# Optimization experiments

Hardware: AMD Instinct MI355X
Metric: run time of the kernel (lower is better)

The kernel has to match this reference:

```python
import jax, jax.numpy as jnp
import numpy as np

B = 16384
D = 64            # bottom_mlp_layers[-1] = embedding_dim
DENSE = 512
HIST = 50         # history length per row
C_CAMP = 1000     # num_collisions for campaign table (sqrt(1e6))
C_FEAT = 316      # num_collisions for 1e5-vocab tables
NQ_CAMP = 1000    # ceil(1e6/1000)
NQ_FEAT = 317     # ceil(1e5/316)
NFEAT = 7
N = NFEAT + 1 + 1 # sparse features + dense row
PROJ = 128


def setup_inputs() -> dict:
    key = jax.random.key(0)
    ks = jax.random.split(key, 20)
    inp = {
        'x': jax.random.normal(ks[0], (B, DENSE), jnp.float32),
        'hist_idx': jax.random.randint(ks[1], (B * HIST,), 0, 1000000),
        'hist_offsets': jnp.arange(B, dtype=jnp.int64) * HIST,
        'feat_idx': jax.random.randint(ks[2], (B, NFEAT), 0, 100000),
        # QR embedding tables (quotient, remainder)
        'Wq_c': jax.random.normal(ks[3], (NQ_CAMP, D), jnp.float32) * 0.05,
        'Wr_c': jax.random.normal(ks[4], (C_CAMP, D), jnp.float32) * 0.05,
        'Wq_f': jax.random.normal(ks[5], (NFEAT, NQ_FEAT, D), jnp.float32) * 0.05,
        'Wr_f': jax.random.normal(ks[6], (NFEAT, C_FEAT, D), jnp.float32) * 0.05,
        # bottom MLP: 512->512 relu 512->256 relu 256->64
        'W0': jax.random.normal(ks[7], (512, DENSE), jnp.float32) * 0.03,
        'b0': jnp.zeros((512,), jnp.float32),
        'W1': jax.random.normal(ks[8], (256, 512), jnp.float32) * 0.04,
        'b1': jnp.zeros((256,), jnp.float32),
        'W2': jax.random.normal(ks[9], (64, 256), jnp.float32) * 0.06,
        'b2': jnp.zeros((64,), jnp.float32),
        # projection: (D + (N^2-N)/2) -> PROJ ; 64 + 36 = 100
        'Wp': jax.random.normal(ks[10], (PROJ, D + (N * N - N) // 2), jnp.float32) * 0.1,
        'bp': jnp.zeros((PROJ,), jnp.float32),
    }
    return inp


def _forward(x, hist_idx, hist_offsets, feat_idx, Wq_c, Wr_c, Wq_f, Wr_f,
             W0, b0, W1, b1, W2, b2, Wp, bp):
    # bottom MLP
    h = jax.nn.relu(x @ W0.T + b0)
    h = jax.nn.relu(h @ W1.T + b1)
    dense = h @ W2.T + b2                                   # [B, D]

    # QR embedding bag (mode='mean', operation='mult') for history feature
    e = Wq_c[hist_idx // C_CAMP] * Wr_c[hist_idx % C_CAMP]  # [M, D]
    M = hist_idx.shape[0]
    seg = jnp.cumsum(jnp.zeros((M,), jnp.int32).at[hist_offsets].add(1)) - 1
    sums = jax.ops.segment_sum(e, seg, num_segments=B)      # [B, D]
    counts = jnp.diff(jnp.concatenate([hist_offsets, jnp.array([M], hist_offsets.dtype)]))
    hist_emb = sums / counts[:, None].astype(sums.dtype)

    # single-valued QR lookups (bag size 1 -> mean == lookup)
    t = jnp.arange(NFEAT)[None, :]
    fe = Wq_f[t, feat_idx // C_FEAT] * Wr_f[t, feat_idx % C_FEAT]  # [B, NFEAT, D]

    # pairwise dot interaction: upper triangle (offset=1) of T @ T^T
    T = jnp.concatenate([dense[:, None, :], hist_emb[:, None, :], fe], axis=1)  # [B, N, D]
    Z = jnp.einsum('bnd,bmd->bnm', T, T)
    row, col = np.triu_indices(N, k=1)
    Z_flat = Z[:, row, col]                                  # [B, (N^2-N)/2]

    combined = jnp.concatenate([dense, Z_flat], axis=1)
    return combined @ Wp.T + bp                              # [B, PROJ]


def reference(x, hist_idx, hist_offsets, feat_idx, Wq_c, Wr_c, Wq_f, Wr_f,
              W0, b0, W1, b1, W2, b2, Wp, bp):
    return _forward(x, hist_idx, hist_offsets, feat_idx, Wq_c, Wr_c, Wq_f, Wr_f,
                    W0, b0, W1, b1, W2, b2, Wp, bp)
```

## Files before the change

### kernel.cpp

```cpp
#include <hip/hip_runtime.h>
#include <hip/hip_bf16.h>
#include <stdint.h>

#define DENSE_D 512
#define HIDDEN1 512
#define HIDDEN2 256
#define EMB_D   64
#define NFEAT   7
#define NROWS   9
#define NPAIRS  36
#define COMB    100
#define KPROJ   128
#define PROJ    128
#define C_CAMP  1000
#define C_FEAT  316
#define NQ_FEAT 317
#define TROWS   16
#define GROWS   8
#define HISTMAX 64

typedef __attribute__((ext_vector_type(8)))  __bf16 bf16x8;
typedef __attribute__((ext_vector_type(8)))  unsigned short ushort8;
typedef __attribute__((ext_vector_type(4)))  float  facc4;

#define GLD_LDS16(gp, lp) __builtin_amdgcn_global_load_lds( \
    (__attribute__((address_space(1))) void*)(gp), \
    (__attribute__((address_space(3))) void*)(lp), 16, 0, 0)

__device__ inline unsigned short f2bf(float f) {
    __hip_bfloat16 h = __float2bfloat16(f);
    return *reinterpret_cast<unsigned short*>(&h);
}
__device__ inline float blo(unsigned int u) { return __uint_as_float(u << 16); }
__device__ inline float bhi(unsigned int u) { return __uint_as_float(u & 0xffff0000u); }

template<int BM, int BN, int BK, int WM, int WN, bool RELU, bool A_F32>
__global__ __launch_bounds__(WM * WN * 64)
void gemm16(const void* __restrict__ Avoid,
            const unsigned short* __restrict__ W,
            const float* __restrict__ bias,
            unsigned short* __restrict__ Cout,
            int M, int N, int K)
{
    constexpr int THREADS = WM * WN * 64;
    constexpr int MREP    = BM / (WM * 16);
    constexpr int NREP    = BN / (WN * 16);
    constexpr int SUB     = BK / 32;
    constexpr int ACH     = BM * BK / 8;
    constexpr int BCH     = BN * BK / 8;

    __shared__ __align__(16) unsigned short Asm[BK / 8][BM][8];
    __shared__ __align__(16) unsigned short Bsm[BK / 8][BN][8];

    const int tid  = threadIdx.x;
    const int lane = tid & 63;
    const int wave = tid >> 6;
    const int wm   = wave / WN;
    const int wn   = wave % WN;
    const int row0 = blockIdx.x * BM;
    const int col0 = blockIdx.y * BN;
    const int fr   = lane & 15;
    const int fk   = lane >> 4;

    facc4 acc[MREP][NREP] = {};

    for (int k0 = 0; k0 < K; k0 += BK) {
        if (A_F32) {
            const float* Af = (const float*)Avoid;
            #pragma unroll
            for (int it = 0; it < ACH / THREADS; ++it) {
                const int p  = it * THREADS + tid;
                const int r  = p & (BM - 1);
                const int kc = p / BM;
                const float* src = Af + (size_t)(row0 + r) * K + k0 + kc * 8;
                const float4 v0 = *reinterpret_cast<const float4*>(src);
                const float4 v1 = *reinterpret_cast<const float4*>(src + 4);
                ushort8 cv;
                cv[0] = f2bf(v0.x); cv[1] = f2bf(v0.y);
                cv[2] = f2bf(v0.z); cv[3] = f2bf(v0.w);
                cv[4] = f2bf(v1.x); cv[5] = f2bf(v1.y);
                cv[6] = f2bf(v1.z); cv[7] = f2bf(v1.w);
                *reinterpret_cast<ushort8*>(
                    (unsigned short*)(&Asm[0][0][0]) + (size_t)p * 8) = cv;
            }
        } else {
            const unsigned short* Ab = (const unsigned short*)Avoid;
            #pragma unroll
            for (int it = 0; it < ACH / THREADS; ++it) {
                const int p  = it * THREADS + tid;
                const int r  = p & (BM - 1);
                const int kc = p / BM;
                GLD_LDS16(Ab + (size_t)(row0 + r) * K + k0 + kc * 8,
                          (&Asm[0][0][0]) + (size_t)p * 8);
            }
        }
        #pragma unroll
        for (int it = 0; it < BCH / THREADS; ++it) {
            const int p  = it * THREADS + tid;
            const int r  = p & (BN - 1);
            const int kc = p / BN;
            GLD_LDS16(W + (size_t)(col0 + r) * K + k0 + kc * 8,
                      (&Bsm[0][0][0]) + (size_t)p * 8);
        }
        __syncthreads();

        #pragma unroll
        for (int s = 0; s < SUB; ++s) {
            bf16x8 af[MREP], bw[NREP];
            #pragma unroll
            for (int m = 0; m < MREP; ++m)
                af[m] = *reinterpret_cast<const bf16x8*>(
                    &Asm[s * 4 + fk][wm * (MREP * 16) + m * 16 + fr][0]);
            #pragma unroll
            for (int n = 0; n < NREP; ++n)
                bw[n] = *reinterpret_cast<const bf16x8*>(
                    &Bsm[s * 4 + fk][wn * (NREP * 16) + n * 16 + fr][0]);
            #pragma unroll
            for (int m = 0; m < MREP; ++m)
                #pragma unroll
                for (int n = 0; n < NREP; ++n)
                    acc[m][n] = __builtin_amdgcn_mfma_f32_16x16x32_bf16(
                        af[m], bw[n], acc[m][n], 0, 0, 0);
        }
        __syncthreads();
    }

    #pragma unroll
    for (int n = 0; n < NREP; ++n) {
        const int col = col0 + wn * (NREP * 16) + n * 16 + fr;
        const float bv = bias[col];
        #pragma unroll
        for (int m = 0; m < MREP; ++m) {
            #pragma unroll
            for (int j = 0; j < 4; ++j) {
                const int row = row0 + wm * (MREP * 16) + m * 16 + fk * 4 + j;
                float v = acc[m][n][j] + bv;
                if (RELU) v = fmaxf(v, 0.f);
                Cout[(size_t)row * N + col] = f2bf(v);
            }
        }
    }
}

__device__ inline void cast_seg(const float* __restrict__ src,
                                unsigned short* __restrict__ dst,
                                int n4, int id, int stride)
{
    for (int i = id; i < n4; i += stride) {
        const float4 v = reinterpret_cast<const float4*>(src)[i];
        ushort4 o;
        o.x = f2bf(v.x); o.y = f2bf(v.y); o.z = f2bf(v.z); o.w = f2bf(v.w);
        reinterpret_cast<ushort4*>(dst)[i] = o;
    }
}

__global__ __launch_bounds__(256)
void prep_all(const float* __restrict__ W0, const float* __restrict__ W1,
              const float* __restrict__ W2, const float* __restrict__ Wp,
              const float* __restrict__ Wq_c, const float* __restrict__ Wr_c,
              const float* __restrict__ Wq_f, const float* __restrict__ Wr_f,
              unsigned short* w0b, unsigned short* w1b, unsigned short* w2b,
              unsigned short* wpb, unsigned short* qcb, unsigned short* rcb,
              unsigned short* qfb, unsigned short* rfb)
{
    const int id = blockIdx.x * blockDim.x + threadIdx.x;
    const int stride = gridDim.x * blockDim.x;
    cast_seg(W0,   w0b, HIDDEN1 * DENSE_D / 4,   id, stride);
    cast_seg(W1,   w1b, HIDDEN2 * HIDDEN1 / 4,   id, stride);
    cast_seg(W2,   w2b, EMB_D * HIDDEN2 / 4,     id, stride);
    cast_seg(Wq_c, qcb, C_CAMP * EMB_D / 4,      id, stride);
    cast_seg(Wr_c, rcb, C_CAMP * EMB_D / 4,      id, stride);
    cast_seg(Wq_f, qfb, NFEAT * NQ_FEAT * EMB_D / 4, id, stride);
    cast_seg(Wr_f, rfb, NFEAT * C_FEAT * EMB_D / 4,  id, stride);
    for (int i = id; i < PROJ * KPROJ; i += stride) {
        const int r = i >> 7, c = i & 127;
        wpb[i] = (c < COMB) ? f2bf(Wp[r * COMB + c]) : (unsigned short)0;
    }
}

__global__ __launch_bounds__(256)
void hist_gather(const int* __restrict__ hist_idx,
                 const int* __restrict__ hist_off,
                 const unsigned short* __restrict__ qcb,
                 const unsigned short* __restrict__ rcb,
                 unsigned short* __restrict__ hemb,
                 int B, int Mtot)
{
    const int r0 = blockIdx.x * GROWS;
    const int t  = threadIdx.x;

    __shared__ int2 soff[GROWS][HISTMAX];
    __shared__ int  scnt[GROWS];

    for (int p = t; p < GROWS * HISTMAX; p += 256) {
        const int row = p >> 6;
        const int i   = p & 63;
        const int br  = r0 + row;
        const int start = hist_off[br];
        const int end   = (br + 1 < B) ? hist_off[br + 1] : Mtot;
        const int cnt   = end - start;
        int2 o = make_int2(0, 0);
        if (i < cnt) {
            const int hi = hist_idx[start + i];
            const int q = hi / C_CAMP;
            o = make_int2(q * EMB_D, (hi - q * C_CAMP) * EMB_D);
        }
        soff[row][i] = o;
        if (i == 0) scnt[row] = cnt;
    }
    __syncthreads();

    const int lane = t & 63;
    const int wv   = t >> 6;
    const int half = lane >> 5;
    const int row  = wv * 2 + half;
    const int l5   = lane & 31;
    const int slot = l5 >> 3;
    const int d8   = l5 & 7;
    const int cnt  = scnt[row];

    const unsigned short* qb = qcb + d8 * 8;
    const unsigned short* rb = rcb + d8 * 8;

    float a[8] = {};
    #define ACC8(q, r) do { \
        a[0] += blo((q).x) * blo((r).x); a[1] += bhi((q).x) * bhi((r).x); \
        a[2] += blo((q).y) * blo((r).y); a[3] += bhi((q).y) * bhi((r).y); \
        a[4] += blo((q).z) * blo((r).z); a[5] += bhi((q).z) * bhi((r).z); \
        a[6] += blo((q).w) * blo((r).w); a[7] += bhi((q).w) * bhi((r).w); } while (0)

    const int full = cnt >> 2;
    int g = 0;
    for (; g + 4 <= full; g += 4) {
        int2 o[4];
        #pragma unroll
        for (int j = 0; j < 4; ++j) o[j] = soff[row][(g + j) * 4 + slot];
        uint4 uq[4], ur[4];
        #pragma unroll
        for (int j = 0; j < 4; ++j) {
            uq[j] = *reinterpret_cast<const uint4*>(qb + o[j].x);
            ur[j] = *reinterpret_cast<const uint4*>(rb + o[j].y);
        }
        #pragma unroll
        for (int j = 0; j < 4; ++j) ACC8(uq[j], ur[j]);
    }
    for (; g < full; ++g) {
        const int2 o = soff[row][g * 4 + slot];
        const uint4 uq = *reinterpret_cast<const uint4*>(qb + o.x);
        const uint4 ur = *reinterpret_cast<const uint4*>(rb + o.y);
        ACC8(uq, ur);
    }
    {
        const int idx = (full << 2) + slot;
        const int2 o = soff[row][idx & (HISTMAX - 1)];
        const uint4 uq = *reinterpret_cast<const uint4*>(qb + o.x);
        const uint4 ur = *reinterpret_cast<const uint4*>(rb + o.y);
        if (idx < cnt) ACC8(uq, ur);
    }
    #undef ACC8

    #pragma unroll
    for (int k = 0; k < 8; ++k) {
        a[k] += __shfl_xor(a[k], 8);
        a[k] += __shfl_xor(a[k], 16);
    }

    if (slot == 0) {
        const float inv = 1.f / (float)max(cnt, 1);
        union { unsigned short s[8]; uint4 u; } pk;
        #pragma unroll
        for (int k = 0; k < 8; ++k) pk.s[k] = f2bf(a[k] * inv);
        *reinterpret_cast<uint4*>(hemb + (size_t)(r0 + row) * EMB_D + d8 * 8) = pk.u;
    }
}

__global__ __launch_bounds__(256)
void tail_rest(const unsigned short* __restrict__ h1b,
               const unsigned short* __restrict__ w2b,
               const float* __restrict__ b2,
               const unsigned short* __restrict__ hemb,
               const int* __restrict__ feat_idx,
               const unsigned short* __restrict__ qfb,
               const unsigned short* __restrict__ rfb,
               const unsigned short* __restrict__ wpb,
               const float* __restrict__ bp,
               float* __restrict__ out)
{
    const int r0   = blockIdx.x * TROWS;
    const int t    = threadIdx.x;
    const int lane = t & 63;
    const int wave = t >> 6;
    const int fr   = lane & 15;
    const int fk   = lane >> 4;

    __shared__ __align__(16) unsigned short T[TROWS][NROWS][72];
    __shared__ __align__(16) unsigned short combs[TROWS][136];

    {
        facc4 acc = {};
        const unsigned short* arow = h1b + (size_t)(r0 + fr) * HIDDEN2;
        const unsigned short* brow = w2b + (size_t)(wave * 16 + fr) * HIDDEN2;
        #pragma unroll
        for (int kw = 0; kw < 8; ++kw) {
            const bf16x8 af = *reinterpret_cast<const bf16x8*>(arow + kw * 32 + fk * 8);
            const bf16x8 bw = *reinterpret_cast<const bf16x8*>(brow + kw * 32 + fk * 8);
            acc = __builtin_amdgcn_mfma_f32_16x16x32_bf16(af, bw, acc, 0, 0, 0);
        }
        const int col = wave * 16 + fr;
        const float bv = b2[col];
        #pragma unroll
        for (int j = 0; j < 4; ++j) {
            const int row = fk * 4 + j;
            const unsigned short hv = f2bf(acc[j] + bv);
            T[row][0][col]  = hv;
            combs[row][col] = hv;
        }
    }

    for (int p = t; p < TROWS * 18; p += 256) {
        const int row = p / 18, c = p % 18;
        *reinterpret_cast<unsigned int*>(&combs[row][100 + c * 2]) = 0u;
    }

    if (t < TROWS * 8) {
        const int row = t >> 3, o8 = t & 7;
        const uint4 v = *reinterpret_cast<const uint4*>(
            hemb + (size_t)(r0 + row) * EMB_D + o8 * 8);
        *reinterpret_cast<uint4*>(&T[row][1][o8 * 8]) = v;
    }

    {
        const int row = t >> 4;
        const int oc  = t & 15;
        const int br  = r0 + row;
        const int fbase = br * NFEAT;
        #pragma unroll
        for (int f = 0; f < NFEAT; ++f) {
            const int fi = feat_idx[fbase + f];
            const int q = fi / C_FEAT, r = fi - q * C_FEAT;
            const uint2 qv = *reinterpret_cast<const uint2*>(
                qfb + ((size_t)f * NQ_FEAT + q) * EMB_D + oc * 4);
            const uint2 rv = *reinterpret_cast<const uint2*>(
                rfb + ((size_t)f * C_FEAT + r) * EMB_D + oc * 4);
            union { ushort4 v; uint2 u; } pk;
            pk.v.x = f2bf(blo(qv.x) * blo(rv.x));
            pk.v.y = f2bf(bhi(qv.x) * bhi(rv.x));
            pk.v.z = f2bf(blo(qv.y) * blo(rv.y));
            pk.v.w = f2bf(bhi(qv.y) * bhi(rv.y));
            *reinterpret_cast<uint2*>(&T[row][2 + f][oc * 4]) = pk.u;
        }
    }
    __syncthreads();

    for (int p = t; p < NPAIRS * TROWS; p += 256) {
        const int row = p & (TROWS - 1);
        const int pr  = p / TROWS;
        int i = 0, rem = pr;
        while (rem >= (NROWS - 1) - i) { rem -= (NROWS - 1) - i; ++i; }
        const int j = i + 1 + rem;
        const unsigned short* ti = &T[row][i][0];
        const unsigned short* tj = &T[row][j][0];
        float s = 0.f;
        #pragma unroll
        for (int d = 0; d < EMB_D; d += 4) {
            const uint2 u = *reinterpret_cast<const uint2*>(ti + d);
            const uint2 v = *reinterpret_cast<const uint2*>(tj + d);
            s += blo(u.x) * blo(v.x) + bhi(u.x) * bhi(v.x)
               + blo(u.y) * blo(v.y) + bhi(u.y) * bhi(v.y);
        }
        combs[row][EMB_D + pr] = f2bf(s);
    }
    __syncthreads();

    {
        facc4 acc[2] = {};
        #pragma unroll
        for (int kw = 0; kw < 4; ++kw) {
            const bf16x8 af = *reinterpret_cast<const bf16x8*>(
                &combs[fr][kw * 32 + fk * 8]);
            #pragma unroll
            for (int n = 0; n < 2; ++n) {
                const bf16x8 bw = *reinterpret_cast<const bf16x8*>(
                    wpb + (size_t)(wave * 32 + n * 16 + fr) * KPROJ + kw * 32 + fk * 8);
                acc[n] = __builtin_amdgcn_mfma_f32_16x16x32_bf16(af, bw, acc[n], 0, 0, 0);
            }
        }
        #pragma unroll
        for (int n = 0; n < 2; ++n) {
            const int col = wave * 32 + n * 16 + fr;
            const float bv = bp[col];
            #pragma unroll
            for (int j = 0; j < 4; ++j) {
                const int row = fk * 4 + j;
                out[(size_t)(r0 + row) * PROJ + col] = acc[n][j] + bv;
            }
        }
    }
}

extern "C" void kernel_launch(void* const* d_in, const int* in_sizes, int n_in,
                              void* d_out, int out_size, void* d_ws, size_t ws_size,
                              hipStream_t stream)
{
    const float* x        = (const float*)d_in[0];
    const int*   hist_idx = (const int*)  d_in[1];
    const int*   hist_off = (const int*)  d_in[2];
    const int*   feat_idx = (const int*)  d_in[3];
    const float* Wq_c     = (const float*)d_in[4];
    const float* Wr_c     = (const float*)d_in[5];
    const float* Wq_f     = (const float*)d_in[6];
    const float* Wr_f     = (const float*)d_in[7];
    const float* W0       = (const float*)d_in[8];
    const float* b0       = (const float*)d_in[9];
    const float* W1       = (const float*)d_in[10];
    const float* b1       = (const float*)d_in[11];
    const float* W2       = (const float*)d_in[12];
    const float* b2       = (const float*)d_in[13];
    const float* Wp       = (const float*)d_in[14];
    const float* bp       = (const float*)d_in[15];

    const int M    = in_sizes[0] / DENSE_D;
    const int Mtot = in_sizes[1];

    char* w = (char*)d_ws;
    auto take = [&](size_t bytes) { char* p = w; w += (bytes + 255) & ~(size_t)255; return p; };
    unsigned short* w0b = (unsigned short*)take(HIDDEN1 * DENSE_D * 2);
    unsigned short* w1b = (unsigned short*)take(HIDDEN2 * HIDDEN1 * 2);
    unsigned short* w2b = (unsigned short*)take(EMB_D * HIDDEN2 * 2);
    unsigned short* wpb = (unsigned short*)take(PROJ * KPROJ * 2);
    unsigned short* qcb = (unsigned short*)take(C_CAMP * EMB_D * 2);
    unsigned short* rcb = (unsigned short*)take(C_CAMP * EMB_D * 2);
    unsigned short* qfb = (unsigned short*)take(NFEAT * NQ_FEAT * EMB_D * 2);
    unsigned short* rfb = (unsigned short*)take(NFEAT * C_FEAT * EMB_D * 2);
    unsigned short* h0b = (unsigned short*)take((size_t)M * HIDDEN1 * 2);
    unsigned short* h1b = (unsigned short*)take((size_t)M * HIDDEN2 * 2);
    unsigned short* hem = (unsigned short*)take((size_t)M * EMB_D * 2);

    prep_all<<<256, 256, 0, stream>>>(W0, W1, W2, Wp, Wq_c, Wr_c, Wq_f, Wr_f,
                                      w0b, w1b, w2b, wpb, qcb, rcb, qfb, rfb);

    hist_gather<<<M / GROWS, 256, 0, stream>>>(
        hist_idx, hist_off, qcb, rcb, hem, M, Mtot);

    gemm16<128, 128, 64, 2, 2, true, true>
        <<<dim3(M / 128, HIDDEN1 / 128), 256, 0, stream>>>(
        x, w0b, b0, h0b, M, HIDDEN1, DENSE_D);

    gemm16<64, 128, 64, 1, 4, true, false>
        <<<dim3(M / 64, HIDDEN2 / 128), 256, 0, stream>>>(
        h0b, w1b, b1, h1b, M, HIDDEN2, HIDDEN1);

    tail_rest<<<M / TROWS, 256, 0, stream>>>(
        h1b, w2b, b2, hem, feat_idx, qfb, rfb, wpb, bp, (float*)d_out);
}
```

Before: 84.57 us.

## Replace multi-wave GEMM tiles with single-wave 64x64 tiles for bottom MLP

Replaces the templated 4-wave GEMM (128x128 and 64x128 tiles with BK=64) with a single-wave kernel that computes a 64x64 tile using BK=32 and a 4x4 grid of MFMA accumulators per wave. This launches many more small blocks and drops the inter-wave split, aiming for more occupancy and better latency hiding through many independent waves. In exchange, each block reuses less data from LDS, so global and L2 traffic for A and W rises, and the K loop takes more iterations with a barrier on each.

```diff
diff --git a/kernel.cpp b/kernel.cpp
--- a/kernel.cpp
+++ b/kernel.cpp
@@ -34,44 +34,33 @@
 __device__ inline float blo(unsigned int u) { return __uint_as_float(u << 16); }
 __device__ inline float bhi(unsigned int u) { return __uint_as_float(u & 0xffff0000u); }
 
-template<int BM, int BN, int BK, int WM, int WN, bool RELU, bool A_F32>
-__global__ __launch_bounds__(WM * WN * 64)
-void gemm16(const void* __restrict__ Avoid,
+template<bool RELU, bool A_F32>
+__global__ __launch_bounds__(64)
+void gemm64(const void* __restrict__ Avoid,
             const unsigned short* __restrict__ W,
             const float* __restrict__ bias,
             unsigned short* __restrict__ Cout,
             int M, int N, int K)
 {
-    constexpr int THREADS = WM * WN * 64;
-    constexpr int MREP    = BM / (WM * 16);
-    constexpr int NREP    = BN / (WN * 16);
-    constexpr int SUB     = BK / 32;
-    constexpr int ACH     = BM * BK / 8;
-    constexpr int BCH     = BN * BK / 8;
-
-    __shared__ __align__(16) unsigned short Asm[BK / 8][BM][8];
-    __shared__ __align__(16) unsigned short Bsm[BK / 8][BN][8];
-
-    const int tid  = threadIdx.x;
-    const int lane = tid & 63;
-    const int wave = tid >> 6;
-    const int wm   = wave / WN;
-    const int wn   = wave % WN;
-    const int row0 = blockIdx.x * BM;
-    const int col0 = blockIdx.y * BN;
+    __shared__ __align__(16) unsigned short Asm[4][64][8];
+    __shared__ __align__(16) unsigned short Bsm[4][64][8];
+
+    const int lane = threadIdx.x;
+    const int row0 = blockIdx.x * 64;
+    const int col0 = blockIdx.y * 64;
     const int fr   = lane & 15;
     const int fk   = lane >> 4;
 
-    facc4 acc[MREP][NREP] = {};
-
-    for (int k0 = 0; k0 < K; k0 += BK) {
+    facc4 acc[4][4] = {};
+
+    for (int k0 = 0; k0 < K; k0 += 32) {
         if (A_F32) {
             const float* Af = (const float*)Avoid;
             #pragma unroll
-            for (int it = 0; it < ACH / THREADS; ++it) {
-                const int p  = it * THREADS + tid;
-                const int r  = p & (BM - 1);
-                const int kc = p / BM;
+            for (int it = 0; it < 4; ++it) {
+                const int p  = it * 64 + lane;
+                const int r  = p & 63;
+                const int kc = p >> 6;
                 const float* src = Af + (size_t)(row0 + r) * K + k0 + kc * 8;
                 const float4 v0 = *reinterpret_cast<const float4*>(src);
                 const float4 v1 = *reinterpret_cast<const float4*>(src + 4);
@@ -86,54 +75,49 @@
         } else {
             const unsigned short* Ab = (const unsigned short*)Avoid;
             #pragma unroll
-            for (int it = 0; it < ACH / THREADS; ++it) {
-                const int p  = it * THREADS + tid;
-                const int r  = p & (BM - 1);
-                const int kc = p / BM;
+            for (int it = 0; it < 4; ++it) {
+                const int p  = it * 64 + lane;
+                const int r  = p & 63;
+                const int kc = p >> 6;
                 GLD_LDS16(Ab + (size_t)(row0 + r) * K + k0 + kc * 8,
                           (&Asm[0][0][0]) + (size_t)p * 8);
             }
         }
         #pragma unroll
-        for (int it = 0; it < BCH / THREADS; ++it) {
-            const int p  = it * THREADS + tid;
-            const int r  = p & (BN - 1);
-            const int kc = p / BN;
+        for (int it = 0; it < 4; ++it) {
+            const int p  = it * 64 + lane;
+            const int r  = p & 63;
+            const int kc = p >> 6;
             GLD_LDS16(W + (size_t)(col0 + r) * K + k0 + kc * 8,
                       (&Bsm[0][0][0]) + (size_t)p * 8);
         }
         __syncthreads();
 
-        #pragma unroll
-        for (int s = 0; s < SUB; ++s) {
-            bf16x8 af[MREP], bw[NREP];
-            #pragma unroll
-            for (int m = 0; m < MREP; ++m)
-                af[m] = *reinterpret_cast<const bf16x8*>(
-                    &Asm[s * 4 + fk][wm * (MREP * 16) + m * 16 + fr][0]);
-            #pragma unroll
-            for (int n = 0; n < NREP; ++n)
-                bw[n] = *reinterpret_cast<const bf16x8*>(
-                    &Bsm[s * 4 + fk][wn * (NREP * 16) + n * 16 + fr][0]);
-            #pragma unroll
-            for (int m = 0; m < MREP; ++m)
-                #pragma unroll
-                for (int n = 0; n < NREP; ++n)
-                    acc[m][n] = __builtin_amdgcn_mfma_f32_16x16x32_bf16(
-                        af[m], bw[n], acc[m][n], 0, 0, 0);
-        }
+        bf16x8 af[4], bw[4];
+        #pragma unroll
+        for (int m = 0; m < 4; ++m)
+            af[m] = *reinterpret_cast<const bf16x8*>(&Asm[fk][m * 16 + fr][0]);
+        #pragma unroll
+        for (int n = 0; n < 4; ++n)
+            bw[n] = *reinterpret_cast<const bf16x8*>(&Bsm[fk][n * 16 + fr][0]);
+        #pragma unroll
+        for (int m = 0; m < 4; ++m)
+            #pragma unroll
+            for (int n = 0; n < 4; ++n)
+                acc[m][n] = __builtin_amdgcn_mfma_f32_16x16x32_bf16(
+                    af[m], bw[n], acc[m][n], 0, 0, 0);
         __syncthreads();
     }
 
     #pragma unroll
-    for (int n = 0; n < NREP; ++n) {
-        const int col = col0 + wn * (NREP * 16) + n * 16 + fr;
+    for (int n = 0; n < 4; ++n) {
+        const int col = col0 + n * 16 + fr;
         const float bv = bias[col];
         #pragma unroll
-        for (int m = 0; m < MREP; ++m) {
+        for (int m = 0; m < 4; ++m) {
             #pragma unroll
             for (int j = 0; j < 4; ++j) {
-                const int row = row0 + wm * (MREP * 16) + m * 16 + fk * 4 + j;
+                const int row = row0 + m * 16 + fk * 4 + j;
                 float v = acc[m][n][j] + bv;
                 if (RELU) v = fmaxf(v, 0.f);
                 Cout[(size_t)row * N + col] = f2bf(v);
@@ -442,12 +426,10 @@
     hist_gather<<<M / GROWS, 256, 0, stream>>>(
         hist_idx, hist_off, qcb, rcb, hem, M, Mtot);
 
-    gemm16<128, 128, 64, 2, 2, true, true>
-        <<<dim3(M / 128, HIDDEN1 / 128), 256, 0, stream>>>(
+    gemm64<true, true><<<dim3(M / 64, HIDDEN1 / 64), 64, 0, stream>>>(
         x, w0b, b0, h0b, M, HIDDEN1, DENSE_D);
 
-    gemm16<64, 128, 64, 1, 4, true, false>
-        <<<dim3(M / 64, HIDDEN2 / 128), 256, 0, stream>>>(
+    gemm64<true, false><<<dim3(M / 64, HIDDEN2 / 64), 64, 0, stream>>>(
         h0b, w1b, b1, h1b, M, HIDDEN2, HIDDEN1);
 
     tail_rest<<<M / TROWS, 256, 0, stream>>>(
```

After: 108.0 us. 27.7% more time.
